# Kernel optimization log

Hardware: AMD Instinct MI355X
Metric: run time of the kernel (lower is better)

The kernel has to match this reference:

```python
import jax, jax.numpy as jnp
import numpy as np

BN_EPS = 1e-5


def setup_inputs() -> dict:
    key = jax.random.key(0)
    ks = jax.random.split(key, 14)
    B, N, C, NS = 2, 1024, 512, 64
    seed_xyz = jax.random.uniform(ks[0], (B, N, 3), jnp.float32)          # points in unit cube
    seed_features = jax.random.normal(ks[1], (B, C, N), jnp.float32)
    # per-seed rotation matrices (orthonormalized via QR)
    rot = jnp.linalg.qr(jax.random.normal(ks[2], (B, N, 3, 3), jnp.float32))[0]
    # cuboid extents sized so each query finds a reasonable neighbor count
    crop_size = 0.2 + 0.3 * jax.random.uniform(ks[3], (B, N, 3), jnp.float32)
    W1 = jax.random.normal(ks[4], (256, 3 + C), jnp.float32) / np.float32(np.sqrt(3 + C))
    gamma1 = 1.0 + 0.1 * jax.random.normal(ks[5], (256,), jnp.float32)
    beta1 = 0.1 * jax.random.normal(ks[6], (256,), jnp.float32)
    mean1 = 0.1 * jax.random.normal(ks[7], (256,), jnp.float32)
    var1 = 0.5 + jax.random.uniform(ks[8], (256,), jnp.float32)
    W2 = jax.random.normal(ks[9], (256, 256), jnp.float32) / np.float32(16.0)
    gamma2 = 1.0 + 0.1 * jax.random.normal(ks[10], (256,), jnp.float32)
    beta2 = 0.1 * jax.random.normal(ks[11], (256,), jnp.float32)
    mean2 = 0.1 * jax.random.normal(ks[12], (256,), jnp.float32)
    var2 = 0.5 + jax.random.uniform(ks[13], (256,), jnp.float32)
    return dict(seed_xyz=seed_xyz, seed_features=seed_features, rot=rot,
                crop_size=crop_size, W1=W1, gamma1=gamma1, beta1=beta1,
                mean1=mean1, var1=var1, W2=W2, gamma2=gamma2, beta2=beta2,
                mean2=mean2, var2=var2, nsample=NS)


def _conv_bn_relu(x, W, g, b, m, v):
    # 1x1 conv (no bias, bn=True) + inference BatchNorm + ReLU
    y = jnp.einsum('bpnc,oc->bpno', x, W)
    scale = g * jax.lax.rsqrt(v + BN_EPS)
    return jax.nn.relu((y - m) * scale + b)


def reference(seed_xyz, seed_features, rot, crop_size,
              W1, gamma1, beta1, mean1, var1,
              W2, gamma2, beta2, mean2, var2, nsample):
    # ---- rotated rectangular query + group (queries == points == seed_xyz) ----
    # diff[b,p,n] = xyz[b,n] - query[b,p]; rotate into the query's local frame
    diff = seed_xyz[:, None, :, :] - seed_xyz[:, :, None, :]          # (B,P,N,3)
    local = jnp.einsum('bpnj,bpjk->bpnk', diff, rot)                  # (B,P,N,3)
    inside = jnp.all(jnp.abs(local) <= 0.5 * crop_size[:, :, None, :], axis=-1)  # (B,P,N)
    # first `nsample` in-region indices, invalid slots filled with the first hit
    order = jnp.argsort(jnp.where(inside, 0, 1).astype(jnp.int32), axis=-1, stable=True)
    idx = order[..., :nsample]                                        # (B,P,NS)
    valid = jnp.take_along_axis(inside, idx, axis=-1)
    idx = jnp.where(valid, idx, idx[..., :1])
    # gather rotated local xyz and features
    g_xyz = jnp.take_along_axis(local, idx[..., None], axis=2)        # (B,P,NS,3)
    feats = jnp.swapaxes(seed_features, 1, 2)                         # (B,N,C)
    g_feat = jax.vmap(lambda f, i: f[i])(feats, idx)                  # (B,P,NS,C)
    grouped = jnp.concatenate([g_xyz, g_feat], axis=-1)               # (B,P,NS,3+C)
    # ---- SharedMLP (1x1 conv + BN + ReLU) x2, then max over samples ----
    h = _conv_bn_relu(grouped, W1, gamma1, beta1, mean1, var1)
    h = _conv_bn_relu(h, W2, gamma2, beta2, mean2, var2)
    out = jnp.max(h, axis=2)                                          # (B,P,256)
    return jnp.swapaxes(out, 1, 2)                                    # (B,256,P)
```

## Files before the change

### kernel.cpp

```cpp
#include <hip/hip_runtime.h>
#include <hip/hip_bf16.h>
#include <math.h>

typedef __attribute__((ext_vector_type(8))) __bf16 bf16x8;
typedef __attribute__((ext_vector_type(4))) __bf16 bf16x4;
typedef __attribute__((ext_vector_type(2))) __bf16 bf16x2;
typedef __attribute__((ext_vector_type(4))) float f32x4;

#define NPTS 1024
#define CIN 512
#define NSAMP 64
#define LDFT 520
#define LDFO 136

__device__ __forceinline__ void local_coords(const float* q, float cx, float cy, float cz,
                                             const float R[9], float& l0, float& l1, float& l2) {
    float d0 = __fsub_rn(q[0], cx);
    float d1 = __fsub_rn(q[1], cy);
    float d2 = __fsub_rn(q[2], cz);
    l0 = __fadd_rn(__fadd_rn(__fmul_rn(d0, R[0]), __fmul_rn(d1, R[3])), __fmul_rn(d2, R[6]));
    l1 = __fadd_rn(__fadd_rn(__fmul_rn(d0, R[1]), __fmul_rn(d1, R[4])), __fmul_rn(d2, R[7]));
    l2 = __fadd_rn(__fadd_rn(__fmul_rn(d0, R[2]), __fmul_rn(d1, R[5])), __fmul_rn(d2, R[8]));
}

__global__ __launch_bounds__(256) void setup_kernel(
    const float* __restrict__ xyz, const float* __restrict__ rot,
    const float* __restrict__ crop,
    const float* __restrict__ W1, const float* __restrict__ W2,
    const float* __restrict__ g1, const float* __restrict__ be1,
    const float* __restrict__ m1, const float* __restrict__ v1,
    const float* __restrict__ g2, const float* __restrict__ be2,
    const float* __restrict__ m2, const float* __restrict__ v2,
    __bf16* __restrict__ W1f, __bf16* __restrict__ W2s,
    float* __restrict__ wxs,
    float* __restrict__ s1, float* __restrict__ b1,
    float* __restrict__ s2, float* __restrict__ b2,
    unsigned short* __restrict__ seln_g, int* __restrict__ cnt_g,
    f32x4* __restrict__ lcsel_g) {
    __shared__ __align__(16) f32x4 lcall[NPTS];
    __shared__ unsigned long long msk[16];
    __shared__ int wpre[17];
    __shared__ int selr[NSAMP];

    const int t = threadIdx.x;
    if (blockIdx.x < 256) {
        const int o = blockIdx.x;
        if (t == 0) {
            float sc1 = g1[o] / sqrtf(v1[o] + 1e-5f);
            s1[o] = sc1;
            b1[o] = be1[o] - m1[o] * sc1;
            float sc2 = g2[o] / sqrtf(v2[o] + 1e-5f);
            s2[o] = sc2;
            b2[o] = be2[o] - m2[o] * sc2;
            wxs[o * 4 + 0] = sc1 * W1[o * 515 + 0];
            wxs[o * 4 + 1] = sc1 * W1[o * 515 + 1];
            wxs[o * 4 + 2] = sc1 * W1[o * 515 + 2];
            wxs[o * 4 + 3] = 0.f;
        }
        for (int k = t; k < CIN; k += blockDim.x)
            W1f[o * CIN + k] = (__bf16)W1[o * 515 + 3 + k];
        {
            const int f = o * 256 + t;
            const int j = f & 7;
            const int l = (f >> 3) & 63;
            const int nt = (f >> 9) & 1;
            const int ks = (f >> 10) & 7;
            const int w = (f >> 13) & 7;
            const int o2 = w * 32 + nt * 16 + (l & 15);
            const int k = ks * 32 + ((l >> 4) << 3) + j;
            W2s[f] = (__bf16)W2[o2 * 256 + k];
        }
        return;
    }
    const int bid = blockIdx.x - 256;
    const int b = bid >> 10;
    const int l = t & 63, w = t >> 6;

    const float cx = xyz[bid * 3 + 0], cy = xyz[bid * 3 + 1], cz = xyz[bid * 3 + 2];
    float R[9];
#pragma unroll
    for (int j = 0; j < 9; ++j) R[j] = rot[bid * 9 + j];
    const float h0 = 0.5f * crop[bid * 3 + 0];
    const float h1 = 0.5f * crop[bid * 3 + 1];
    const float h2 = 0.5f * crop[bid * 3 + 2];

#pragma unroll
    for (int i = 0; i < 4; ++i) {
        const int n = i * 256 + t;
        float l0, l1, l2;
        local_coords(xyz + (size_t)(b * NPTS + n) * 3, cx, cy, cz, R, l0, l1, l2);
        lcall[n] = f32x4{l0, l1, l2, 0.f};
        bool ins = (__builtin_fabsf(l0) <= h0) && (__builtin_fabsf(l1) <= h1) &&
                   (__builtin_fabsf(l2) <= h2);
        unsigned long long bal = __ballot(ins);
        if (l == 0) msk[i * 4 + w] = bal;
    }
    __syncthreads();
    if (t < 64) {
        const int c = (t < 16) ? __popcll(msk[t]) : 0;
        int sum = c;
#pragma unroll
        for (int d = 1; d < 16; d <<= 1) {
            int v = __shfl_up(sum, d);
            if (t >= d) sum += v;
        }
        if (t < 16) wpre[t] = sum - c;
        if (t == 15) wpre[16] = sum;
    }
    __syncthreads();
    const int cnt = wpre[16];
#pragma unroll
    for (int i = 0; i < 4; ++i) {
        const int n = i * 256 + t;
        const unsigned long long wd = msk[n >> 6];
        const int bit = n & 63;
        if ((wd >> bit) & 1ull) {
            int rank = wpre[n >> 6] + __popcll(wd & ((1ull << bit) - 1ull));
            if (rank < NSAMP) selr[rank] = n;
        }
    }
    __syncthreads();
    if (t < NSAMP) {
        const int n = selr[(t < cnt) ? t : 0];
        seln_g[(size_t)bid * NSAMP + t] = (unsigned short)n;
        lcsel_g[(size_t)bid * NSAMP + t] = lcall[n];
    }
    if (t == 0) cnt_g[bid] = cnt;
}

__global__ __launch_bounds__(256) void fgemm_kernel(const float* __restrict__ feats,
                                                    const __bf16* __restrict__ W1f,
                                                    const float* __restrict__ s1,
                                                    const float* __restrict__ b1,
                                                    __bf16* __restrict__ Fsb) {
    __shared__ __align__(16) __bf16 Ft[16][LDFT];
    __shared__ __align__(16) __bf16 Fo[16][LDFO];
    const int t = threadIdx.x;
    const int b = blockIdx.x >> 7;
    const int half = (blockIdx.x >> 6) & 1;
    const int n0 = (blockIdx.x & 63) << 4;
    const int l = t & 63, w = t >> 6;
    const int lo = l & 15, kg = l >> 4;

    const float* fb = feats + (size_t)b * (CIN * NPTS) + n0;
    {
        const int n = t & 15;
        const int cq = (t >> 4) * 2;
        for (int i = 0; i < 16; ++i) {
            int c = i * 32 + cq;
            float v0 = fb[(size_t)c * NPTS + n];
            float v1v = fb[(size_t)(c + 1) * NPTS + n];
            bf16x2 pk = {(__bf16)v0, (__bf16)v1v};
            *(bf16x2*)(&Ft[n][c]) = pk;
        }
    }
    __syncthreads();

    f32x4 acc[2];
#pragma unroll
    for (int mt = 0; mt < 2; ++mt) acc[mt] = f32x4{0.f, 0.f, 0.f, 0.f};

#pragma unroll
    for (int ks = 0; ks < 16; ++ks) {
        const int kk = ks * 32 + kg * 8;
        const bf16x8 bfr = *(const bf16x8*)(&Ft[lo][kk]);
#pragma unroll
        for (int mt = 0; mt < 2; ++mt) {
            const int o = half * 128 + w * 32 + mt * 16 + lo;
            const bf16x8 af = *(const bf16x8*)(&W1f[(size_t)o * CIN + kk]);
            acc[mt] = __builtin_amdgcn_mfma_f32_16x16x32_bf16(af, bfr, acc[mt], 0, 0, 0);
        }
    }
    __syncthreads();
#pragma unroll
    for (int mt = 0; mt < 2; ++mt) {
        const int ol = w * 32 + mt * 16 + kg * 4;
        const f32x4 sv = *(const f32x4*)(&s1[half * 128 + ol]);
        const f32x4 bv = *(const f32x4*)(&b1[half * 128 + ol]);
        bf16x4 r;
#pragma unroll
        for (int j = 0; j < 4; ++j) r[j] = (__bf16)fmaf(acc[mt][j], sv[j], bv[j]);
        *(bf16x4*)(&Fo[lo][ol]) = r;
    }
    __syncthreads();
    {
        const int row = t >> 4, c = t & 15;
        const bf16x8 v = *(const bf16x8*)(&Fo[row][c * 8]);
        *(bf16x8*)(&Fsb[((size_t)(b * NPTS + n0 + row)) * 256 + half * 128 + c * 8]) = v;
    }
}

__global__ __launch_bounds__(512, 2) void fused_kernel(
    const __bf16* __restrict__ Fsb, const float* __restrict__ wxs,
    const unsigned short* __restrict__ seln_g, const int* __restrict__ cnt_g,
    const f32x4* __restrict__ lcsel_g,
    const __bf16* __restrict__ W2s, const float* __restrict__ s2g, const float* __restrict__ b2g,
    float* __restrict__ out) {
    __shared__ __align__(16) char A2raw[NSAMP * 512];
    __shared__ __align__(16) f32x4 lcL[8][NSAMP];
    __shared__ __align__(16) float outst[256][8];
    __shared__ unsigned short selL[8][NSAMP];
    __shared__ int cntL[8];

    const int raw = (int)blockIdx.x;
    const int pg = (raw & 7) * 32 + (raw >> 3);
    const int b = pg >> 7;
    const int p0 = (pg & 127) * 8;
    const int t = threadIdx.x;
    const int l = t & 63, w = t >> 6;
    const int lo = l & 15, kg = l >> 4;

    {
        const int pi = t >> 6, s = t & 63;
        const size_t base = ((size_t)(b * NPTS + p0 + pi)) * NSAMP + s;
        selL[pi][s] = seln_g[base];
        lcL[pi][s] = lcsel_g[base];
    }
    if (t < 8) cntL[t] = cnt_g[b * NPTS + p0 + t];

    bf16x8 wf[8][2];
#pragma unroll
    for (int ks = 0; ks < 8; ++ks)
#pragma unroll
        for (int nt = 0; nt < 2; ++nt)
            wf[ks][nt] = *(const bf16x8*)(&W2s[(size_t)((((w * 8 + ks) * 2 + nt) * 64) + l) * 8]);

    const int oc4 = (t & 63) * 4;
    const int g8 = t >> 6;
    f32x4 wv4[4];
#pragma unroll
    for (int j = 0; j < 4; ++j) wv4[j] = *(const f32x4*)(&wxs[(oc4 + j) * 4]);

    float sc[2], bb[2];
#pragma unroll
    for (int nt = 0; nt < 2; ++nt) {
        const int o = w * 32 + nt * 16 + lo;
        sc[nt] = s2g[o];
        bb[nt] = b2g[o];
    }
    __syncthreads();

    bf16x4 stg[8];
    {
        const int rpad = (min(cntL[0], NSAMP) + 15) & ~15;
#pragma unroll
        for (int si = 0; si < 8; ++si) {
            const int s = g8 * 8 + si;
            if (s < rpad) {
                const int n = (int)selL[0][s];
                stg[si] = *(const bf16x4*)(&Fsb[((size_t)(b * NPTS + n)) * 256 + oc4]);
            }
        }
#pragma unroll
        for (int si = 0; si < 8; ++si) {
            const int s = g8 * 8 + si;
            if (s < rpad) {
                const f32x4 cd = lcL[0][s];
#pragma unroll
                for (int j = 0; j < 4; ++j) {
                    const float x = fmaf(cd.x, wv4[j].x,
                                         fmaf(cd.y, wv4[j].y,
                                              fmaf(cd.z, wv4[j].z, (float)stg[si][j])));
                    stg[si][j] = (__bf16)fmaxf(x, 0.f);
                }
                *(bf16x4*)(A2raw + s * 512 + ((oc4 * 2) ^ ((s & 7) << 4))) = stg[si];
            }
        }
    }
    __syncthreads();

    for (int pi = 0; pi < 8; ++pi) {
        const int mtmax = (min(cntL[pi], NSAMP) + 15) >> 4;
        int rpadn = 0;
        if (pi < 7) {
            rpadn = (min(cntL[pi + 1], NSAMP) + 15) & ~15;
#pragma unroll
            for (int si = 0; si < 8; ++si) {
                const int s = g8 * 8 + si;
                if (s < rpadn) {
                    const int n = (int)selL[pi + 1][s];
                    stg[si] = *(const bf16x4*)(&Fsb[((size_t)(b * NPTS + n)) * 256 + oc4]);
                }
            }
        }

        f32x4 acc[4][2];
#pragma unroll
        for (int mt = 0; mt < 4; ++mt)
#pragma unroll
            for (int nt = 0; nt < 2; ++nt)
                acc[mt][nt] = f32x4{0.f, 0.f, 0.f, 0.f};

#pragma unroll
        for (int mt = 0; mt < 4; ++mt) {
            if (mt < mtmax) {
                const int row = mt * 16 + lo;
#pragma unroll
                for (int ks = 0; ks < 8; ++ks) {
                    const bf16x8 a = *(const bf16x8*)(A2raw + row * 512 +
                                                      ((ks * 64 + kg * 16) ^ ((row & 7) << 4)));
                    acc[mt][0] = __builtin_amdgcn_mfma_f32_16x16x32_bf16(a, wf[ks][0],
                                                                         acc[mt][0], 0, 0, 0);
                    acc[mt][1] = __builtin_amdgcn_mfma_f32_16x16x32_bf16(a, wf[ks][1],
                                                                         acc[mt][1], 0, 0, 0);
                }
            }
        }

        if (pi < 7) {
#pragma unroll
            for (int si = 0; si < 8; ++si) {
                const int s = g8 * 8 + si;
                if (s < rpadn) {
                    const f32x4 cd = lcL[pi + 1][s];
#pragma unroll
                    for (int j = 0; j < 4; ++j) {
                        const float x = fmaf(cd.x, wv4[j].x,
                                             fmaf(cd.y, wv4[j].y,
                                                  fmaf(cd.z, wv4[j].z, (float)stg[si][j])));
                        stg[si][j] = (__bf16)fmaxf(x, 0.f);
                    }
                }
            }
        }

#pragma unroll
        for (int nt = 0; nt < 2; ++nt) {
            float mx = 0.f;
#pragma unroll
            for (int mt = 0; mt < 4; ++mt) {
                if (mt < mtmax) {
#pragma unroll
                    for (int r = 0; r < 4; ++r)
                        mx = fmaxf(mx, fmaxf(fmaf(acc[mt][nt][r], sc[nt], bb[nt]), 0.f));
                }
            }
            mx = fmaxf(mx, __shfl_xor(mx, 16));
            mx = fmaxf(mx, __shfl_xor(mx, 32));
            if (kg == 0) outst[w * 32 + nt * 16 + lo][pi] = mx;
        }
        __syncthreads();

        if (pi < 7) {
#pragma unroll
            for (int si = 0; si < 8; ++si) {
                const int s = g8 * 8 + si;
                if (s < rpadn)
                    *(bf16x4*)(A2raw + s * 512 + ((oc4 * 2) ^ ((s & 7) << 4))) = stg[si];
            }
        }
        __syncthreads();
    }

    {
        const int o = t >> 1, hf = t & 1;
        const f32x4 v = *(const f32x4*)(&outst[o][hf * 4]);
        *(f32x4*)(&out[((size_t)b * 256 + o) * NPTS + p0 + hf * 4]) = v;
    }
}

extern "C" void kernel_launch(void* const* d_in, const int* in_sizes, int n_in,
                              void* d_out, int out_size, void* d_ws, size_t ws_size,
                              hipStream_t stream) {
    (void)in_sizes; (void)n_in; (void)out_size; (void)ws_size;
    const float* xyz   = (const float*)d_in[0];
    const float* feats = (const float*)d_in[1];
    const float* rot   = (const float*)d_in[2];
    const float* crop  = (const float*)d_in[3];
    const float* W1    = (const float*)d_in[4];
    const float* g1    = (const float*)d_in[5];
    const float* be1   = (const float*)d_in[6];
    const float* m1    = (const float*)d_in[7];
    const float* v1    = (const float*)d_in[8];
    const float* W2    = (const float*)d_in[9];
    const float* g2    = (const float*)d_in[10];
    const float* be2   = (const float*)d_in[11];
    const float* m2    = (const float*)d_in[12];
    const float* v2    = (const float*)d_in[13];

    char* ws = (char*)d_ws;
    __bf16* W1f = (__bf16*)(ws + 0);
    __bf16* W2s = (__bf16*)(ws + 262144);
    float*  wxs = (float*)(ws + 393216);
    float*  s1  = (float*)(ws + 397312);
    float*  b1  = (float*)(ws + 398336);
    float*  s2  = (float*)(ws + 399360);
    float*  b2  = (float*)(ws + 400384);
    __bf16* Fsb = (__bf16*)(ws + 401408);
    unsigned short* seln = (unsigned short*)(ws + 1449984);
    int*    cntg = (int*)(ws + 1712128);
    f32x4*  lcse = (f32x4*)(ws + 1720320);

    setup_kernel<<<2304, 256, 0, stream>>>(xyz, rot, crop,
                                           W1, W2, g1, be1, m1, v1, g2, be2, m2, v2,
                                           W1f, W2s, wxs, s1, b1, s2, b2, seln, cntg, lcse);
    fgemm_kernel<<<256, 256, 0, stream>>>(feats, W1f, s1, b1, Fsb);
    fused_kernel<<<256, 512, 0, stream>>>(Fsb, wxs, seln, cntg, lcse, W2s, s2, b2,
                                          (float*)d_out);
}
```

Before: 44.16 us.

## Process two query points per iteration with 2D warp tiling over samples and outputs

```diff
diff --git a/kernel.cpp b/kernel.cpp
--- a/kernel.cpp
+++ b/kernel.cpp
@@ -63,10 +63,10 @@
             const int f = o * 256 + t;
             const int j = f & 7;
             const int l = (f >> 3) & 63;
-            const int nt = (f >> 9) & 1;
-            const int ks = (f >> 10) & 7;
-            const int w = (f >> 13) & 7;
-            const int o2 = w * 32 + nt * 16 + (l & 15);
+            const int nt = (f >> 9) & 3;
+            const int ks = (f >> 11) & 7;
+            const int oh = (f >> 14) & 3;
+            const int o2 = oh * 64 + nt * 16 + (l & 15);
             const int k = ks * 32 + ((l >> 4) << 3) + j;
             W2s[f] = (__bf16)W2[o2 * 256 + k];
         }
@@ -196,9 +196,9 @@
     const f32x4* __restrict__ lcsel_g,
     const __bf16* __restrict__ W2s, const float* __restrict__ s2g, const float* __restrict__ b2g,
     float* __restrict__ out) {
-    __shared__ __align__(16) char A2raw[NSAMP * 512];
+    __shared__ __align__(16) char A2raw[2][NSAMP * 512];
     __shared__ __align__(16) f32x4 lcL[8][NSAMP];
-    __shared__ __align__(16) float outst[256][8];
+    __shared__ __align__(16) float outst2[2][256][8];
     __shared__ unsigned short selL[8][NSAMP];
     __shared__ int cntL[8];
 
@@ -209,6 +209,7 @@
     const int t = threadIdx.x;
     const int l = t & 63, w = t >> 6;
     const int lo = l & 15, kg = l >> 4;
+    const int oh = w & 3, sh = w >> 2;
 
     {
         const int pi = t >> 6, s = t & 63;
@@ -218,12 +219,12 @@
     }
     if (t < 8) cntL[t] = cnt_g[b * NPTS + p0 + t];
 
-    bf16x8 wf[8][2];
+    bf16x8 wf[8][4];
 #pragma unroll
     for (int ks = 0; ks < 8; ++ks)
 #pragma unroll
-        for (int nt = 0; nt < 2; ++nt)
-            wf[ks][nt] = *(const bf16x8*)(&W2s[(size_t)((((w * 8 + ks) * 2 + nt) * 64) + l) * 8]);
+        for (int nt = 0; nt < 4; ++nt)
+            wf[ks][nt] = *(const bf16x8*)(&W2s[(size_t)((((oh * 8 + ks) * 4 + nt) * 64) + l) * 8]);
 
     const int oc4 = (t & 63) * 4;
     const int g8 = t >> 6;
@@ -231,122 +232,170 @@
 #pragma unroll
     for (int j = 0; j < 4; ++j) wv4[j] = *(const f32x4*)(&wxs[(oc4 + j) * 4]);
 
-    float sc[2], bb[2];
-#pragma unroll
-    for (int nt = 0; nt < 2; ++nt) {
-        const int o = w * 32 + nt * 16 + lo;
+    float sc[4], bb[4];
+#pragma unroll
+    for (int nt = 0; nt < 4; ++nt) {
+        const int o = oh * 64 + nt * 16 + lo;
         sc[nt] = s2g[o];
         bb[nt] = b2g[o];
     }
     __syncthreads();
 
-    bf16x4 stg[8];
+    bf16x4 stgA[8], stgB[8];
+
     {
-        const int rpad = (min(cntL[0], NSAMP) + 15) & ~15;
+        const int rpad0 = (min(cntL[0], NSAMP) + 15) & ~15;
+        const int rpad1 = (min(cntL[1], NSAMP) + 15) & ~15;
 #pragma unroll
         for (int si = 0; si < 8; ++si) {
             const int s = g8 * 8 + si;
-            if (s < rpad) {
-                const int n = (int)selL[0][s];
-                stg[si] = *(const bf16x4*)(&Fsb[((size_t)(b * NPTS + n)) * 256 + oc4]);
-            }
+            if (s < rpad0)
+                stgA[si] = *(const bf16x4*)(&Fsb[((size_t)(b * NPTS + (int)selL[0][s])) * 256 + oc4]);
+            if (s < rpad1)
+                stgB[si] = *(const bf16x4*)(&Fsb[((size_t)(b * NPTS + (int)selL[1][s])) * 256 + oc4]);
         }
 #pragma unroll
         for (int si = 0; si < 8; ++si) {
             const int s = g8 * 8 + si;
-            if (s < rpad) {
+            if (s < rpad0) {
                 const f32x4 cd = lcL[0][s];
 #pragma unroll
                 for (int j = 0; j < 4; ++j) {
                     const float x = fmaf(cd.x, wv4[j].x,
-                                         fmaf(cd.y, wv4[j].y,
-                                              fmaf(cd.z, wv4[j].z, (float)stg[si][j])));
-                    stg[si][j] = (__bf16)fmaxf(x, 0.f);
-                }
-                *(bf16x4*)(A2raw + s * 512 + ((oc4 * 2) ^ ((s & 7) << 4))) = stg[si];
-            }
-        }
-    }
-    __syncthreads();
-
-    for (int pi = 0; pi < 8; ++pi) {
-        const int mtmax = (min(cntL[pi], NSAMP) + 15) >> 4;
-        int rpadn = 0;
-        if (pi < 7) {
-            rpadn = (min(cntL[pi + 1], NSAMP) + 15) & ~15;
+                                         fmaf(cd.y, wv4[j].y, fmaf(cd.z, wv4[j].z, (float)stgA[si][j])));
+                    stgA[si][j] = (__bf16)fmaxf(x, 0.f);
+                }
+                *(bf16x4*)(A2raw[0] + s * 512 + ((oc4 * 2) ^ ((s & 7) << 4))) = stgA[si];
+            }
+            if (s < rpad1) {
+                const f32x4 cd = lcL[1][s];
+#pragma unroll
+                for (int j = 0; j < 4; ++j) {
+                    const float x = fmaf(cd.x, wv4[j].x,
+                                         fmaf(cd.y, wv4[j].y, fmaf(cd.z, wv4[j].z, (float)stgB[si][j])));
+                    stgB[si][j] = (__bf16)fmaxf(x, 0.f);
+                }
+                *(bf16x4*)(A2raw[1] + s * 512 + ((oc4 * 2) ^ ((s & 7) << 4))) = stgB[si];
+            }
+        }
+    }
+    __syncthreads();
+
+    for (int pp = 0; pp < 4; ++pp) {
+        const int mt0 = (min(cntL[pp * 2], NSAMP) + 15) >> 4;
+        const int mt1 = (min(cntL[pp * 2 + 1], NSAMP) + 15) >> 4;
+        int rpA = 0, rpB = 0;
+        if (pp < 3) {
+            rpA = (min(cntL[pp * 2 + 2], NSAMP) + 15) & ~15;
+            rpB = (min(cntL[pp * 2 + 3], NSAMP) + 15) & ~15;
 #pragma unroll
             for (int si = 0; si < 8; ++si) {
                 const int s = g8 * 8 + si;
-                if (s < rpadn) {
-                    const int n = (int)selL[pi + 1][s];
-                    stg[si] = *(const bf16x4*)(&Fsb[((size_t)(b * NPTS + n)) * 256 + oc4]);
-                }
-            }
-        }
-
-        f32x4 acc[4][2];
-#pragma unroll
-        for (int mt = 0; mt < 4; ++mt)
-#pragma unroll
-            for (int nt = 0; nt < 2; ++nt)
-                acc[mt][nt] = f32x4{0.f, 0.f, 0.f, 0.f};
-
-#pragma unroll
-        for (int mt = 0; mt < 4; ++mt) {
-            if (mt < mtmax) {
-                const int row = mt * 16 + lo;
+                if (s < rpA)
+                    stgA[si] = *(const bf16x4*)(&Fsb[((size_t)(b * NPTS + (int)selL[pp * 2 + 2][s])) * 256 + oc4]);
+                if (s < rpB)
+                    stgB[si] = *(const bf16x4*)(&Fsb[((size_t)(b * NPTS + (int)selL[pp * 2 + 3][s])) * 256 + oc4]);
+            }
+        }
+
+        f32x4 acc0[2][4], acc1[2][4];
+#pragma unroll
+        for (int mt = 0; mt < 2; ++mt)
+#pragma unroll
+            for (int nt = 0; nt < 4; ++nt) {
+                acc0[mt][nt] = f32x4{0.f, 0.f, 0.f, 0.f};
+                acc1[mt][nt] = f32x4{0.f, 0.f, 0.f, 0.f};
+            }
+
+#pragma unroll
+        for (int mt = 0; mt < 2; ++mt) {
+            const int tidx = sh * 2 + mt;
+            const int row = sh * 32 + mt * 16 + lo;
+            if (tidx < mt0) {
 #pragma unroll
                 for (int ks = 0; ks < 8; ++ks) {
-                    const bf16x8 a = *(const bf16x8*)(A2raw + row * 512 +
+                    const bf16x8 a = *(const bf16x8*)(A2raw[0] + row * 512 +
                                                       ((ks * 64 + kg * 16) ^ ((row & 7) << 4)));
-                    acc[mt][0] = __builtin_amdgcn_mfma_f32_16x16x32_bf16(a, wf[ks][0],
-                                                                         acc[mt][0], 0, 0, 0);
-                    acc[mt][1] = __builtin_amdgcn_mfma_f32_16x16x32_bf16(a, wf[ks][1],
-                                                                         acc[mt][1], 0, 0, 0);
-                }
-            }
-        }
-
-        if (pi < 7) {
+#pragma unroll
+                    for (int nt = 0; nt < 4; ++nt)
+                        acc0[mt][nt] = __builtin_amdgcn_mfma_f32_16x16x32_bf16(a, wf[ks][nt],
+                                                                               acc0[mt][nt], 0, 0, 0);
+                }
+            }
+            if (tidx < mt1) {
+#pragma unroll
+                for (int ks = 0; ks < 8; ++ks) {
+                    const bf16x8 a = *(const bf16x8*)(A2raw[1] + row * 512 +
+                                                      ((ks * 64 + kg * 16) ^ ((row & 7) << 4)));
+#pragma unroll
+                    for (int nt = 0; nt < 4; ++nt)
+                        acc1[mt][nt] = __builtin_amdgcn_mfma_f32_16x16x32_bf16(a, wf[ks][nt],
+                                                                               acc1[mt][nt], 0, 0, 0);
+                }
+            }
+        }
+
+        if (pp < 3) {
 #pragma unroll
             for (int si = 0; si < 8; ++si) {
                 const int s = g8 * 8 + si;
-                if (s < rpadn) {
-                    const f32x4 cd = lcL[pi + 1][s];
+                if (s < rpA) {
+                    const f32x4 cd = lcL[pp * 2 + 2][s];
 #pragma unroll
                     for (int j = 0; j < 4; ++j) {
                         const float x = fmaf(cd.x, wv4[j].x,
-                                             fmaf(cd.y, wv4[j].y,
-                                                  fmaf(cd.z, wv4[j].z, (float)stg[si][j])));
-                        stg[si][j] = (__bf16)fmaxf(x, 0.f);
+                                             fmaf(cd.y, wv4[j].y, fmaf(cd.z, wv4[j].z, (float)stgA[si][j])));
+                        stgA[si][j] = (__bf16)fmaxf(x, 0.f);
                     }
                 }
-            }
-        }
-
-#pragma unroll
-        for (int nt = 0; nt < 2; ++nt) {
-            float mx = 0.f;
-#pragma unroll
-            for (int mt = 0; mt < 4; ++mt) {
-                if (mt < mtmax) {
+                if (s < rpB) {
+                    const f32x4 cd = lcL[pp * 2 + 3][s];
+#pragma unroll
+                    for (int j = 0; j < 4; ++j) {
+                        const float x = fmaf(cd.x, wv4[j].x,
+                                             fmaf(cd.y, wv4[j].y, fmaf(cd.z, wv4[j].z, (float)stgB[si][j])));
+                        stgB[si][j] = (__bf16)fmaxf(x, 0.f);
+                    }
+                }
+            }
+        }
+
+#pragma unroll
+        for (int nt = 0; nt < 4; ++nt) {
+            float mx0 = 0.f, mx1 = 0.f;
+#pragma unroll
+            for (int mt = 0; mt < 2; ++mt) {
+                const int tidx = sh * 2 + mt;
+                if (tidx < mt0) {
 #pragma unroll
                     for (int r = 0; r < 4; ++r)
-                        mx = fmaxf(mx, fmaxf(fmaf(acc[mt][nt][r], sc[nt], bb[nt]), 0.f));
-                }
-            }
-            mx = fmaxf(mx, __shfl_xor(mx, 16));
-            mx = fmaxf(mx, __shfl_xor(mx, 32));
-            if (kg == 0) outst[w * 32 + nt * 16 + lo][pi] = mx;
+                        mx0 = fmaxf(mx0, fmaxf(fmaf(acc0[mt][nt][r], sc[nt], bb[nt]), 0.f));
+                }
+                if (tidx < mt1) {
+#pragma unroll
+                    for (int r = 0; r < 4; ++r)
+                        mx1 = fmaxf(mx1, fmaxf(fmaf(acc1[mt][nt][r], sc[nt], bb[nt]), 0.f));
+                }
+            }
+            mx0 = fmaxf(mx0, __shfl_xor(mx0, 16));
+            mx0 = fmaxf(mx0, __shfl_xor(mx0, 32));
+            mx1 = fmaxf(mx1, __shfl_xor(mx1, 16));
+            mx1 = fmaxf(mx1, __shfl_xor(mx1, 32));
+            if (kg == 0) {
+                outst2[sh][oh * 64 + nt * 16 + lo][pp * 2 + 0] = mx0;
+                outst2[sh][oh * 64 + nt * 16 + lo][pp * 2 + 1] = mx1;
+            }
         }
         __syncthreads();
 
-        if (pi < 7) {
+        if (pp < 3) {
 #pragma unroll
             for (int si = 0; si < 8; ++si) {
                 const int s = g8 * 8 + si;
-                if (s < rpadn)
-                    *(bf16x4*)(A2raw + s * 512 + ((oc4 * 2) ^ ((s & 7) << 4))) = stg[si];
+                if (s < rpA)
+                    *(bf16x4*)(A2raw[0] + s * 512 + ((oc4 * 2) ^ ((s & 7) << 4))) = stgA[si];
+                if (s < rpB)
+                    *(bf16x4*)(A2raw[1] + s * 512 + ((oc4 * 2) ^ ((s & 7) << 4))) = stgB[si];
             }
         }
         __syncthreads();
@@ -354,8 +403,14 @@
 
     {
         const int o = t >> 1, hf = t & 1;
-        const f32x4 v = *(const f32x4*)(&outst[o][hf * 4]);
-        *(f32x4*)(&out[((size_t)b * 256 + o) * NPTS + p0 + hf * 4]) = v;
+        if (t < 512) {
+            const f32x4 v0 = *(const f32x4*)(&outst2[0][o][hf * 4]);
+            const f32x4 v1 = *(const f32x4*)(&outst2[1][o][hf * 4]);
+            f32x4 v;
+#pragma unroll
+            for (int j = 0; j < 4; ++j) v[j] = fmaxf(v0[j], v1[j]);
+            *(f32x4*)(&out[((size_t)b * 256 + o) * NPTS + p0 + hf * 4]) = v;
+        }
     }
 }
 
```

Result: slower. 67.39 us (+52.6%).

## Batch four query points per phase to cut barriers in fused MLP kernel

Applied to the files above, without the earlier changes.

```diff
diff --git a/kernel.cpp b/kernel.cpp
--- a/kernel.cpp
+++ b/kernel.cpp
@@ -196,7 +196,7 @@
     const f32x4* __restrict__ lcsel_g,
     const __bf16* __restrict__ W2s, const float* __restrict__ s2g, const float* __restrict__ b2g,
     float* __restrict__ out) {
-    __shared__ __align__(16) char A2raw[NSAMP * 512];
+    __shared__ __align__(16) char A2raw[4 * NSAMP * 512];
     __shared__ __align__(16) f32x4 lcL[8][NSAMP];
     __shared__ __align__(16) float outst[256][8];
     __shared__ unsigned short selL[8][NSAMP];
@@ -240,64 +240,66 @@
     }
     __syncthreads();
 
-    bf16x4 stg[8];
-    {
-        const int rpad = (min(cntL[0], NSAMP) + 15) & ~15;
+    bf16x4 stg[4][8];
+    int rp[4];
+
+#pragma unroll
+    for (int pl = 0; pl < 4; ++pl) {
+        rp[pl] = (min(cntL[pl], NSAMP) + 15) & ~15;
 #pragma unroll
         for (int si = 0; si < 8; ++si) {
             const int s = g8 * 8 + si;
-            if (s < rpad) {
-                const int n = (int)selL[0][s];
-                stg[si] = *(const bf16x4*)(&Fsb[((size_t)(b * NPTS + n)) * 256 + oc4]);
-            }
-        }
+            if (s < rp[pl])
+                stg[pl][si] = *(const bf16x4*)(&Fsb[((size_t)(b * NPTS + (int)selL[pl][s])) * 256 + oc4]);
+        }
+    }
+#pragma unroll
+    for (int pl = 0; pl < 4; ++pl) {
 #pragma unroll
         for (int si = 0; si < 8; ++si) {
             const int s = g8 * 8 + si;
-            if (s < rpad) {
-                const f32x4 cd = lcL[0][s];
+            if (s < rp[pl]) {
+                const f32x4 cd = lcL[pl][s];
+                bf16x4 r = stg[pl][si];
 #pragma unroll
                 for (int j = 0; j < 4; ++j) {
                     const float x = fmaf(cd.x, wv4[j].x,
-                                         fmaf(cd.y, wv4[j].y,
-                                              fmaf(cd.z, wv4[j].z, (float)stg[si][j])));
-                    stg[si][j] = (__bf16)fmaxf(x, 0.f);
-                }
-                *(bf16x4*)(A2raw + s * 512 + ((oc4 * 2) ^ ((s & 7) << 4))) = stg[si];
-            }
-        }
-    }
-    __syncthreads();
-
-    for (int pi = 0; pi < 8; ++pi) {
-        const int mtmax = (min(cntL[pi], NSAMP) + 15) >> 4;
-        int rpadn = 0;
-        if (pi < 7) {
-            rpadn = (min(cntL[pi + 1], NSAMP) + 15) & ~15;
-#pragma unroll
-            for (int si = 0; si < 8; ++si) {
-                const int s = g8 * 8 + si;
-                if (s < rpadn) {
-                    const int n = (int)selL[pi + 1][s];
-                    stg[si] = *(const bf16x4*)(&Fsb[((size_t)(b * NPTS + n)) * 256 + oc4]);
-                }
-            }
-        }
-
+                                         fmaf(cd.y, wv4[j].y, fmaf(cd.z, wv4[j].z, (float)r[j])));
+                    r[j] = (__bf16)fmaxf(x, 0.f);
+                }
+                *(bf16x4*)(A2raw + (pl * NSAMP + s) * 512 + ((oc4 * 2) ^ ((s & 7) << 4))) = r;
+            }
+        }
+    }
+    int rp1[4];
+#pragma unroll
+    for (int pl = 0; pl < 4; ++pl) {
+        rp1[pl] = (min(cntL[4 + pl], NSAMP) + 15) & ~15;
+#pragma unroll
+        for (int si = 0; si < 8; ++si) {
+            const int s = g8 * 8 + si;
+            if (s < rp1[pl])
+                stg[pl][si] = *(const bf16x4*)(&Fsb[((size_t)(b * NPTS + (int)selL[4 + pl][s])) * 256 + oc4]);
+        }
+    }
+    __syncthreads();
+
+#pragma unroll
+    for (int pl = 0; pl < 4; ++pl) {
+        const int mtmax = (min(cntL[pl], NSAMP) + 15) >> 4;
         f32x4 acc[4][2];
 #pragma unroll
         for (int mt = 0; mt < 4; ++mt)
 #pragma unroll
             for (int nt = 0; nt < 2; ++nt)
                 acc[mt][nt] = f32x4{0.f, 0.f, 0.f, 0.f};
-
 #pragma unroll
         for (int mt = 0; mt < 4; ++mt) {
             if (mt < mtmax) {
                 const int row = mt * 16 + lo;
 #pragma unroll
                 for (int ks = 0; ks < 8; ++ks) {
-                    const bf16x8 a = *(const bf16x8*)(A2raw + row * 512 +
+                    const bf16x8 a = *(const bf16x8*)(A2raw + (pl * NSAMP + row) * 512 +
                                                       ((ks * 64 + kg * 16) ^ ((row & 7) << 4)));
                     acc[mt][0] = __builtin_amdgcn_mfma_f32_16x16x32_bf16(a, wf[ks][0],
                                                                          acc[mt][0], 0, 0, 0);
@@ -306,24 +308,6 @@
                 }
             }
         }
-
-        if (pi < 7) {
-#pragma unroll
-            for (int si = 0; si < 8; ++si) {
-                const int s = g8 * 8 + si;
-                if (s < rpadn) {
-                    const f32x4 cd = lcL[pi + 1][s];
-#pragma unroll
-                    for (int j = 0; j < 4; ++j) {
-                        const float x = fmaf(cd.x, wv4[j].x,
-                                             fmaf(cd.y, wv4[j].y,
-                                                  fmaf(cd.z, wv4[j].z, (float)stg[si][j])));
-                        stg[si][j] = (__bf16)fmaxf(x, 0.f);
-                    }
-                }
-            }
-        }
-
 #pragma unroll
         for (int nt = 0; nt < 2; ++nt) {
             float mx = 0.f;
@@ -337,20 +321,72 @@
             }
             mx = fmaxf(mx, __shfl_xor(mx, 16));
             mx = fmaxf(mx, __shfl_xor(mx, 32));
-            if (kg == 0) outst[w * 32 + nt * 16 + lo][pi] = mx;
-        }
-        __syncthreads();
-
-        if (pi < 7) {
-#pragma unroll
-            for (int si = 0; si < 8; ++si) {
-                const int s = g8 * 8 + si;
-                if (s < rpadn)
-                    *(bf16x4*)(A2raw + s * 512 + ((oc4 * 2) ^ ((s & 7) << 4))) = stg[si];
-            }
-        }
-        __syncthreads();
-    }
+            if (kg == 0) outst[w * 32 + nt * 16 + lo][pl] = mx;
+        }
+    }
+    __syncthreads();
+
+#pragma unroll
+    for (int pl = 0; pl < 4; ++pl) {
+#pragma unroll
+        for (int si = 0; si < 8; ++si) {
+            const int s = g8 * 8 + si;
+            if (s < rp1[pl]) {
+                const f32x4 cd = lcL[4 + pl][s];
+                bf16x4 r = stg[pl][si];
+#pragma unroll
+                for (int j = 0; j < 4; ++j) {
+                    const float x = fmaf(cd.x, wv4[j].x,
+                                         fmaf(cd.y, wv4[j].y, fmaf(cd.z, wv4[j].z, (float)r[j])));
+                    r[j] = (__bf16)fmaxf(x, 0.f);
+                }
+                *(bf16x4*)(A2raw + (pl * NSAMP + s) * 512 + ((oc4 * 2) ^ ((s & 7) << 4))) = r;
+            }
+        }
+    }
+    __syncthreads();
+
+#pragma unroll
+    for (int pl = 0; pl < 4; ++pl) {
+        const int mtmax = (min(cntL[4 + pl], NSAMP) + 15) >> 4;
+        f32x4 acc[4][2];
+#pragma unroll
+        for (int mt = 0; mt < 4; ++mt)
+#pragma unroll
+            for (int nt = 0; nt < 2; ++nt)
+                acc[mt][nt] = f32x4{0.f, 0.f, 0.f, 0.f};
+#pragma unroll
+        for (int mt = 0; mt < 4; ++mt) {
+            if (mt < mtmax) {
+                const int row = mt * 16 + lo;
+#pragma unroll
+                for (int ks = 0; ks < 8; ++ks) {
+                    const bf16x8 a = *(const bf16x8*)(A2raw + (pl * NSAMP + row) * 512 +
+                                                      ((ks * 64 + kg * 16) ^ ((row & 7) << 4)));
+                    acc[mt][0] = __builtin_amdgcn_mfma_f32_16x16x32_bf16(a, wf[ks][0],
+                                                                         acc[mt][0], 0, 0, 0);
+                    acc[mt][1] = __builtin_amdgcn_mfma_f32_16x16x32_bf16(a, wf[ks][1],
+                                                                         acc[mt][1], 0, 0, 0);
+                }
+            }
+        }
+#pragma unroll
+        for (int nt = 0; nt < 2; ++nt) {
+            float mx = 0.f;
+#pragma unroll
+            for (int mt = 0; mt < 4; ++mt) {
+                if (mt < mtmax) {
+#pragma unroll
+                    for (int r = 0; r < 4; ++r)
+                        mx = fmaxf(mx, fmaxf(fmaf(acc[mt][nt][r], sc[nt], bb[nt]), 0.f));
+                }
+            }
+            mx = fmaxf(mx, __shfl_xor(mx, 16));
+            mx = fmaxf(mx, __shfl_xor(mx, 32));
+            if (kg == 0) outst[w * 32 + nt * 16 + lo][4 + pl] = mx;
+        }
+    }
+    __syncthreads();
 
     {
         const int o = t >> 1, hf = t & 1;
```

Result: faster. 42.91 us, median of 2 (-2.8%).
